# Kernel optimization log

Hardware: AMD Instinct MI355X
Metric: run time of the kernel (lower is better)

The kernel has to match this reference:

```python
import jax, jax.numpy as jnp
import numpy as np

EPS = 1e-6


def setup_inputs() -> dict:
    key = jax.random.key(0)
    k1, k2, k3, k4 = jax.random.split(key, 4)
    B, N, D = 8, 4096, 512
    x = jax.random.normal(k1, (B, N, D), dtype=jnp.float32)
    # torch nn.Linear(dim, 3*dim, bias=False): weight shape [3D, D], y = x @ W.T
    w_qkv = jax.random.normal(k2, (3 * D, D), dtype=jnp.float32) * (1.0 / np.sqrt(D))
    w_proj = jax.random.normal(k3, (D, D), dtype=jnp.float32) * (1.0 / np.sqrt(D))
    b_proj = jax.random.normal(k4, (D,), dtype=jnp.float32) * 0.01
    return {"x": x, "w_qkv": w_qkv, "w_proj": w_proj, "b_proj": b_proj, "heads": 8}


def reference(x, w_qkv, w_proj, b_proj, heads):
    B, N, D = x.shape
    H = heads
    d = D // H
    # qkv projection -> (3, B, H, N, d)
    qkv = (x @ w_qkv.T).reshape(B, N, 3, H, d).transpose(2, 0, 3, 1, 4)
    q, k, v = qkv[0], qkv[1], qkv[2]
    # elu+1 feature map (positive features)
    q = jax.nn.elu(q) + 1.0 + EPS
    k = jax.nn.elu(k) + 1.0 + EPS
    # kv summary: [B,H,d,d]
    kv = jnp.einsum('bhnd,bhne->bhde', k, v)
    # denominator: q . sum_n(k) -> [B,H,N]
    denom = jnp.einsum('bhnd,bhd->bhn', q, k.sum(axis=2))
    out = jnp.einsum('bhnd,bhde->bhne', q, kv) / (denom[..., None] + EPS)
    out = out.transpose(0, 2, 1, 3).reshape(B, N, D)
    return out @ w_proj.T + b_proj
```

## Files before the change

kernel.cpp:

```cpp
#include <hip/hip_runtime.h>
#include <hip/hip_bf16.h>
#include <math.h>

#define EPSF 1e-6f

constexpr int Bc = 8;
constexpr int Nc = 4096;
constexpr int Dc = 512;
constexpr int QKVC = 3 * Dc;

typedef __attribute__((ext_vector_type(8))) short short8v;
typedef __attribute__((ext_vector_type(8))) unsigned short ushort8v;
typedef __attribute__((ext_vector_type(4))) float float4v;

__device__ __forceinline__ unsigned short f2bf(float f) {
    union { float f; unsigned int u; } v; v.f = f;
    unsigned int u = v.u;
    return (unsigned short)((u + 0x7fffu + ((u >> 16) & 1u)) >> 16);
}
__device__ __forceinline__ float bf2f(unsigned short h) {
    union { unsigned int u; float f; } v; v.u = ((unsigned int)h) << 16;
    return v.f;
}

typedef __attribute__((address_space(1))) const void gvoid_t;
typedef __attribute__((address_space(3))) void lvoid_t;
__device__ __forceinline__ void llds16(const void* g, void* l) {
    __builtin_amdgcn_global_load_lds((gvoid_t*)g, (lvoid_t*)l, 16, 0, 0);
}

__global__ __launch_bounds__(256) void cvt_f32_bf16(
    const float* __restrict__ in, unsigned short* __restrict__ out, int n8)
{
    int i = blockIdx.x * 256 + threadIdx.x;
    if (i >= n8) return;
    float4 a = reinterpret_cast<const float4*>(in)[2 * i];
    float4 b = reinterpret_cast<const float4*>(in)[2 * i + 1];
    ushort8v o;
    o[0] = f2bf(a.x); o[1] = f2bf(a.y); o[2] = f2bf(a.z); o[3] = f2bf(a.w);
    o[4] = f2bf(b.x); o[5] = f2bf(b.y); o[6] = f2bf(b.z); o[7] = f2bf(b.w);
    reinterpret_cast<ushort8v*>(out)[i] = o;
}

__global__ __launch_bounds__(256) void cvt_weights(
    const float* __restrict__ wq, const float* __restrict__ wp,
    unsigned short* __restrict__ wqo, unsigned short* __restrict__ wpo)
{
    const int i = blockIdx.x * 256 + threadIdx.x;
    const int NQ = 1536 * 512 / 8;
    const float* src; unsigned short* dst; int idx;
    if (i < NQ) { src = wq; dst = wqo; idx = i; }
    else        { src = wp; dst = wpo; idx = i - NQ; }
    float4 a = reinterpret_cast<const float4*>(src)[2 * idx];
    float4 b = reinterpret_cast<const float4*>(src)[2 * idx + 1];
    ushort8v o;
    o[0] = f2bf(a.x); o[1] = f2bf(a.y); o[2] = f2bf(a.z); o[3] = f2bf(a.w);
    o[4] = f2bf(b.x); o[5] = f2bf(b.y); o[6] = f2bf(b.z); o[7] = f2bf(b.w);
    reinterpret_cast<ushort8v*>(dst)[idx] = o;
}

__global__ __launch_bounds__(512, 2) void gemm_qkv(
    const unsigned short* __restrict__ A,
    const unsigned short* __restrict__ Bm,
    unsigned short* __restrict__ Cout)
{
    constexpr int LDA = 512, LDB = 512, LDC = 1536;
    constexpr int NT = 8;
    __shared__ unsigned short ring[3][24576];

    const int t = threadIdx.x;
    const int orig = blockIdx.x;
    const int wg = (orig & 7) * 192 + (orig >> 3);
    const int bm = (wg / 12) * 256;
    const int bn = (wg % 12) * 128;

    const int w = t >> 6, lane = t & 63;
    const int ln = lane & 15, g = lane >> 4;
    const int wr = (w >> 1) * 64;
    const int wc = (w & 1) * 64;
    const int l7 = ln & 7;

    const int rs = t >> 3;
    const int ci = t & 7;
    const int swz = ci ^ (rs & 7);
    const unsigned short* As0 = A + (size_t)(bm + rs) * LDA + swz * 8;
    const unsigned short* As1 = A + (size_t)(bm + 64 + rs) * LDA + swz * 8;
    const unsigned short* As2 = A + (size_t)(bm + 128 + rs) * LDA + swz * 8;
    const unsigned short* As3 = A + (size_t)(bm + 192 + rs) * LDA + swz * 8;
    const unsigned short* Bs0 = Bm + (size_t)(bn + rs) * LDB + swz * 8;
    const unsigned short* Bs1 = Bm + (size_t)(bn + 64 + rs) * LDB + swz * 8;

#define STAGEQ(Tt) do {                                                        \
        const int k0_ = (Tt) * 64;                                             \
        unsigned short* dA_ = &ring[(Tt) % 3][0];                              \
        unsigned short* dB_ = &ring[(Tt) % 3][16384];                          \
        llds16(As0 + k0_, dA_ + (size_t)t * 8);                                \
        llds16(As1 + k0_, dA_ + (size_t)(512 + t) * 8);                        \
        llds16(As2 + k0_, dA_ + (size_t)(1024 + t) * 8);                       \
        llds16(As3 + k0_, dA_ + (size_t)(1536 + t) * 8);                       \
        llds16(Bs0 + k0_, dB_ + (size_t)t * 8);                                \
        llds16(Bs1 + k0_, dB_ + (size_t)(512 + t) * 8);                        \
    } while (0)

    float4v acc[4][4];
#pragma unroll
    for (int i = 0; i < 4; ++i)
#pragma unroll
        for (int j = 0; j < 4; ++j) acc[i][j] = {0.f, 0.f, 0.f, 0.f};

    STAGEQ(0);
    STAGEQ(1);
    asm volatile("s_waitcnt vmcnt(6)" ::: "memory");
    __builtin_amdgcn_s_barrier();
    __builtin_amdgcn_sched_barrier(0);

#pragma unroll
    for (int T = 0; T < NT; ++T) {
        if (T + 2 < NT) STAGEQ(T + 2);

        const unsigned short* base = &ring[T % 3][0];
        short8v a[4][2], b[4][2];
#pragma unroll
        for (int i = 0; i < 4; ++i)
#pragma unroll
            for (int kk = 0; kk < 2; ++kk) {
                const int row = wr + i * 16 + ln;
                a[i][kk] = *reinterpret_cast<const short8v*>(
                    base + row * 64 + (((kk * 4 + g) ^ l7) << 3));
            }
#pragma unroll
        for (int j = 0; j < 4; ++j)
#pragma unroll
            for (int kk = 0; kk < 2; ++kk) {
                const int row = wc + j * 16 + ln;
                b[j][kk] = *reinterpret_cast<const short8v*>(
                    base + 16384 + row * 64 + (((kk * 4 + g) ^ l7) << 3));
            }

        __builtin_amdgcn_s_setprio(1);
#pragma unroll
        for (int kk = 0; kk < 2; ++kk)
#pragma unroll
            for (int i = 0; i < 4; ++i)
#pragma unroll
                for (int j = 0; j < 4; ++j)
                    acc[i][j] = __builtin_amdgcn_mfma_f32_16x16x32_bf16(
                        a[i][kk], b[j][kk], acc[i][j], 0, 0, 0);
        __builtin_amdgcn_s_setprio(0);

        if (T + 1 < NT) {
            if (T + 2 < NT)
                asm volatile("s_waitcnt vmcnt(6)" ::: "memory");
            else
                asm volatile("s_waitcnt vmcnt(0)" ::: "memory");
            __builtin_amdgcn_s_barrier();
            __builtin_amdgcn_sched_barrier(0);
        }
    }
#undef STAGEQ

#pragma unroll
    for (int i = 0; i < 4; ++i) {
        const int Rb = bm + wr + i * 16 + g * 4;
#pragma unroll
        for (int j = 0; j < 4; ++j) {
            const int Cc = bn + wc + j * 16 + ln;
            const bool do_elu = (Cc < 1024);
#pragma unroll
            for (int r = 0; r < 4; ++r) {
                float v = acc[i][j][r];
                if (do_elu) v = (v > 0.f) ? (v + 1.0f + EPSF) : (expf(v) + EPSF);
                Cout[(size_t)(Rb + r) * LDC + Cc] = f2bf(v);
            }
        }
    }
}

__global__ __launch_bounds__(256) void kv_part(
    const unsigned short* __restrict__ qkv,
    float* __restrict__ kvp, float* __restrict__ ksp)
{
    const int bh = blockIdx.x, chunk = blockIdx.y;
    const int b = bh >> 3, h = bh & 7;

    __shared__ float ktT[4096];
    __shared__ float vtT[4096];
    __shared__ float ksl[16][64];

    const int t = threadIdx.x;
    const int di = t >> 4, ej = t & 15;
    const bool isK = (t < 128);
    const int ts = isK ? t : t - 128;
    const int slot = ts & 7;
    const int ng = ts >> 3;

    const size_t base = ((size_t)b * Nc + (size_t)chunk * 512) * QKVC + h * 64
                      + (isK ? Dc : 2 * Dc) + slot * 8;

    float acc[4][4] = {};
    float ks8[8] = {};

    for (int it = 0; it < 8; ++it) {
        {
            const unsigned short* src = qkv + base + (size_t)(it * 64 + 4 * ng) * QKVC;
            ushort8v r0 = *reinterpret_cast<const ushort8v*>(src);
            ushort8v r1 = *reinterpret_cast<const ushort8v*>(src + QKVC);
            ushort8v r2 = *reinterpret_cast<const ushort8v*>(src + 2 * QKVC);
            ushort8v r3 = *reinterpret_cast<const ushort8v*>(src + 3 * QKVC);
            float* dst = isK ? ktT : vtT;
#pragma unroll
            for (int i = 0; i < 8; ++i) {
                const int row = 8 * slot + i;
                float4 wv = make_float4(bf2f(r0[i]), bf2f(r1[i]), bf2f(r2[i]), bf2f(r3[i]));
                *reinterpret_cast<float4*>(dst + row * 64 + ((ng ^ (row & 15)) << 2)) = wv;
                if (isK) ks8[i] += wv.x + wv.y + wv.z + wv.w;
            }
        }
        __syncthreads();

#pragma unroll 4
        for (int nc = 0; nc < 16; ++nc) {
            float4 kd[4], ve[4];
#pragma unroll
            for (int i = 0; i < 4; ++i)
                kd[i] = *reinterpret_cast<const float4*>(
                    ktT + (di + 16 * i) * 64 + ((nc ^ di) << 2));
#pragma unroll
            for (int j = 0; j < 4; ++j)
                ve[j] = *reinterpret_cast<const float4*>(
                    vtT + (ej + 16 * j) * 64 + ((nc ^ ej) << 2));
#pragma unroll
            for (int i = 0; i < 4; ++i)
#pragma unroll
                for (int j = 0; j < 4; ++j) {
                    acc[i][j] += kd[i].x * ve[j].x;
                    acc[i][j] += kd[i].y * ve[j].y;
                    acc[i][j] += kd[i].z * ve[j].z;
                    acc[i][j] += kd[i].w * ve[j].w;
                }
        }
        __syncthreads();
    }

    float* kvpp = kvp + ((size_t)bh * 8 + chunk) * 4096;
#pragma unroll
    for (int i = 0; i < 4; ++i)
#pragma unroll
        for (int j = 0; j < 4; ++j)
            kvpp[(di + 16 * i) * 64 + (ej + 16 * j)] = acc[i][j];

    if (isK) {
#pragma unroll
        for (int i = 0; i < 8; ++i) ksl[ng][8 * slot + i] = ks8[i];
    }
    __syncthreads();
    if (t < 64) {
        float s = 0.f;
#pragma unroll
        for (int c = 0; c < 16; ++c) s += ksl[c][t];
        ksp[((size_t)bh * 8 + chunk) * 64 + t] = s;
    }
}

__global__ __launch_bounds__(256) void kv_reduce(
    const float* __restrict__ kvp, const float* __restrict__ ksp,
    unsigned short* __restrict__ kvb, float* __restrict__ ksum)
{
    const int bh = blockIdx.x, t = threadIdx.x;
    const float* src = kvp + (size_t)bh * 8 * 4096;
#pragma unroll
    for (int i = 0; i < 16; ++i) {
        const int idx = i * 256 + t;
        float s = 0.f;
#pragma unroll
        for (int c = 0; c < 8; ++c) s += src[c * 4096 + idx];
        kvb[(size_t)bh * 4096 + idx] = f2bf(s);
    }
    if (t < 64) {
        float s = 0.f;
#pragma unroll
        for (int c = 0; c < 8; ++c) s += ksp[((size_t)bh * 8 + c) * 64 + t];
        ksum[bh * 64 + t] = s;
    }
}

__global__ __launch_bounds__(256) void gemm_M(
    const unsigned short* __restrict__ kvb,
    const unsigned short* __restrict__ wp,
    unsigned short* __restrict__ MT)
{
    const int bh = blockIdx.x, b = bh >> 3, h = bh & 7;
    const int t = threadIdx.x, w = t >> 6, lane = t & 63;
    const int ln = lane & 15, g = lane >> 4;

    float4v acc[8][4];
#pragma unroll
    for (int i = 0; i < 8; ++i)
#pragma unroll
        for (int j = 0; j < 4; ++j) acc[i][j] = {0.f, 0.f, 0.f, 0.f};

#pragma unroll
    for (int kk = 0; kk < 2; ++kk) {
        short8v a[8], bf[4];
#pragma unroll
        for (int i = 0; i < 8; ++i)
            a[i] = *reinterpret_cast<const short8v*>(
                wp + (size_t)(w * 128 + i * 16 + ln) * 512 + h * 64 + kk * 32 + g * 8);
#pragma unroll
        for (int j = 0; j < 4; ++j)
            bf[j] = *reinterpret_cast<const short8v*>(
                kvb + (size_t)bh * 4096 + (j * 16 + ln) * 64 + kk * 32 + g * 8);
#pragma unroll
        for (int i = 0; i < 8; ++i)
#pragma unroll
            for (int j = 0; j < 4; ++j)
                acc[i][j] = __builtin_amdgcn_mfma_f32_16x16x32_bf16(a[i], bf[j], acc[i][j], 0, 0, 0);
    }

#pragma unroll
    for (int i = 0; i < 8; ++i) {
        const int c0 = w * 128 + i * 16 + g * 4;
#pragma unroll
        for (int j = 0; j < 4; ++j) {
            const int d = j * 16 + ln;
#pragma unroll
            for (int r = 0; r < 4; ++r)
                MT[(size_t)b * 262144 + (size_t)(c0 + r) * 512 + h * 64 + d] =
                    f2bf(acc[i][j][r]);
        }
    }
}

__global__ __launch_bounds__(256) void q_scale(
    unsigned short* __restrict__ qkv, const float* __restrict__ ksum)
{
    __shared__ float kss[512];
    const int blk = blockIdx.x;
    const int b = blk >> 7;
    const int t = threadIdx.x;
    kss[t] = ksum[b * 512 + t];
    kss[t + 256] = ksum[b * 512 + 256 + t];
    __syncthreads();

    const int row = blk * 32 + (t >> 3);
    const int h = t & 7;
    unsigned short* p = qkv + (size_t)row * QKVC + h * 64;

    ushort8v v[8];
#pragma unroll
    for (int s = 0; s < 8; ++s) v[s] = *reinterpret_cast<const ushort8v*>(p + s * 8);

    float den = EPSF;
#pragma unroll
    for (int s = 0; s < 8; ++s)
#pragma unroll
        for (int m = 0; m < 8; ++m)
            den += bf2f(v[s][m]) * kss[h * 64 + s * 8 + m];
    const float inv = 1.0f / den;

#pragma unroll
    for (int s = 0; s < 8; ++s) {
        ushort8v o;
#pragma unroll
        for (int m = 0; m < 8; ++m) o[m] = f2bf(bf2f(v[s][m]) * inv);
        *reinterpret_cast<ushort8v*>(p + s * 8) = o;
    }
}

__global__ __launch_bounds__(512, 2) void gemm_out(
    const unsigned short* __restrict__ A,
    const unsigned short* __restrict__ Bt,
    const float* __restrict__ bias,
    float* __restrict__ out)
{
    constexpr int LDA = 1536, LDB = 512, NT = 8;
    __shared__ unsigned short ring[3][24576];

    const int t = threadIdx.x;
    const int orig = blockIdx.x;
    const int wg = (orig & 7) * 64 + (orig >> 3);
    const int bm = (wg >> 2) * 256;
    const int bn = (wg & 3) * 128;
    const unsigned short* Bm = Bt + (size_t)(bm >> 12) * 262144;

    const int w = t >> 6, lane = t & 63;
    const int ln = lane & 15, g = lane >> 4;
    const int wr = (w >> 1) * 64;
    const int wc = (w & 1) * 64;
    const int l7 = ln & 7;

    const int rs = t >> 3;
    const int ci = t & 7;
    const int swz = ci ^ (rs & 7);
    const unsigned short* As0 = A + (size_t)(bm + rs) * LDA + swz * 8;
    const unsigned short* As1 = A + (size_t)(bm + 64 + rs) * LDA + swz * 8;
    const unsigned short* As2 = A + (size_t)(bm + 128 + rs) * LDA + swz * 8;
    const unsigned short* As3 = A + (size_t)(bm + 192 + rs) * LDA + swz * 8;
    const unsigned short* Bs0 = Bm + (size_t)(bn + rs) * LDB + swz * 8;
    const unsigned short* Bs1 = Bm + (size_t)(bn + 64 + rs) * LDB + swz * 8;

#define STAGEO(Tt) do {                                                        \
        const int k0_ = (Tt) * 64;                                             \
        unsigned short* dA_ = &ring[(Tt) % 3][0];                              \
        unsigned short* dB_ = &ring[(Tt) % 3][16384];                          \
        llds16(As0 + k0_, dA_ + (size_t)t * 8);                                \
        llds16(As1 + k0_, dA_ + (size_t)(512 + t) * 8);                        \
        llds16(As2 + k0_, dA_ + (size_t)(1024 + t) * 8);                       \
        llds16(As3 + k0_, dA_ + (size_t)(1536 + t) * 8);                       \
        llds16(Bs0 + k0_, dB_ + (size_t)t * 8);                                \
        llds16(Bs1 + k0_, dB_ + (size_t)(512 + t) * 8);                        \
    } while (0)

    float4v acc[4][4];
#pragma unroll
    for (int i = 0; i < 4; ++i)
#pragma unroll
        for (int j = 0; j < 4; ++j) acc[i][j] = {0.f, 0.f, 0.f, 0.f};

    STAGEO(0);
    STAGEO(1);
    asm volatile("s_waitcnt vmcnt(6)" ::: "memory");
    __builtin_amdgcn_s_barrier();
    __builtin_amdgcn_sched_barrier(0);

#pragma unroll
    for (int T = 0; T < NT; ++T) {
        if (T + 2 < NT) STAGEO(T + 2);

        const unsigned short* base = &ring[T % 3][0];
        short8v a[4][2], b[4][2];
#pragma unroll
        for (int i = 0; i < 4; ++i)
#pragma unroll
            for (int kk = 0; kk < 2; ++kk) {
                const int row = wr + i * 16 + ln;
                a[i][kk] = *reinterpret_cast<const short8v*>(
                    base + row * 64 + (((kk * 4 + g) ^ l7) << 3));
            }
#pragma unroll
        for (int j = 0; j < 4; ++j)
#pragma unroll
            for (int kk = 0; kk < 2; ++kk) {
                const int row = wc + j * 16 + ln;
                b[j][kk] = *reinterpret_cast<const short8v*>(
                    base + 16384 + row * 64 + (((kk * 4 + g) ^ l7) << 3));
            }

        __builtin_amdgcn_s_setprio(1);
#pragma unroll
        for (int kk = 0; kk < 2; ++kk)
#pragma unroll
            for (int i = 0; i < 4; ++i)
#pragma unroll
                for (int j = 0; j < 4; ++j)
                    acc[i][j] = __builtin_amdgcn_mfma_f32_16x16x32_bf16(
                        a[i][kk], b[j][kk], acc[i][j], 0, 0, 0);
        __builtin_amdgcn_s_setprio(0);

        if (T + 1 < NT) {
            if (T + 2 < NT)
                asm volatile("s_waitcnt vmcnt(6)" ::: "memory");
            else
                asm volatile("s_waitcnt vmcnt(0)" ::: "memory");
            __builtin_amdgcn_s_barrier();
            __builtin_amdgcn_sched_barrier(0);
        }
    }
#undef STAGEO

#pragma unroll
    for (int i = 0; i < 4; ++i) {
        const int Rb = bm + wr + i * 16 + g * 4;
#pragma unroll
        for (int j = 0; j < 4; ++j) {
            const int Cc = bn + wc + j * 16 + ln;
            const float bv = bias[Cc];
#pragma unroll
            for (int r = 0; r < 4; ++r)
                out[(size_t)(Rb + r) * 512 + Cc] = acc[i][j][r] + bv;
        }
    }
}

extern "C" void kernel_launch(void* const* d_in, const int* in_sizes, int n_in,
                              void* d_out, int out_size, void* d_ws, size_t ws_size,
                              hipStream_t stream)
{
    const float* x      = (const float*)d_in[0];
    const float* w_qkv  = (const float*)d_in[1];
    const float* w_proj = (const float*)d_in[2];
    const float* b_proj = (const float*)d_in[3];
    float* out = (float*)d_out;

    char* ws = (char*)d_ws;
    unsigned short* qkvb = (unsigned short*)ws;
    size_t off = (size_t)32768 * 1536 * 2;
    unsigned short* xb   = (unsigned short*)(ws + off); off += (size_t)32768 * 512 * 2;
    unsigned short* wqb  = (unsigned short*)(ws + off); off += (size_t)1536 * 512 * 2;
    unsigned short* wpb  = (unsigned short*)(ws + off); off += (size_t)512 * 512 * 2;
    float* kvp           = (float*)(ws + off);          off += (size_t)64 * 8 * 4096 * 4;
    float* ksp           = (float*)(ws + off);          off += (size_t)64 * 8 * 64 * 4;
    unsigned short* kvb  = (unsigned short*)(ws + off); off += (size_t)64 * 4096 * 2;
    float* ksumb         = (float*)(ws + off);          off += (size_t)64 * 64 * 4;
    unsigned short* MT   = (unsigned short*)(ws + off); off += (size_t)8 * 512 * 512 * 2;

    cvt_f32_bf16<<<dim3((32768 * 512 / 8 + 255) / 256), dim3(256), 0, stream>>>(x, xb, 32768 * 512 / 8);
    cvt_weights<<<dim3(((1536 * 512 + 512 * 512) / 8 + 255) / 256), dim3(256), 0, stream>>>(
        w_qkv, w_proj, wqb, wpb);

    gemm_qkv<<<dim3(1536), dim3(512), 0, stream>>>(xb, wqb, qkvb);

    kv_part<<<dim3(64, 8), dim3(256), 0, stream>>>(qkvb, kvp, ksp);
    kv_reduce<<<dim3(64), dim3(256), 0, stream>>>(kvp, ksp, kvb, ksumb);

    gemm_M<<<dim3(64), dim3(256), 0, stream>>>(kvb, wpb, MT);

    q_scale<<<dim3(1024), dim3(256), 0, stream>>>(qkvb, ksumb);

    gemm_out<<<dim3(512), dim3(512), 0, stream>>>(qkvb, MT, b_proj, out);
}
```

Baseline: 199.0 us.

## Compute kv partial products with bf16 MFMA instead of scalar FMA

The kv_part kernel now stores K and V tiles in shared memory as bf16, with padded rows in place of float XOR-swizzled rows. Each wavefront computes a 16x64 slice of the 64x64 K^T V partial using mfma_f32_16x16x32_bf16 rather than a 4x4-per-thread FP32 outer-product loop. This halves the LDS footprint and removes the scalar FMA work. Numerics should match closely, since the inputs were already bf16 and accumulation stays in fp32. kv_part is only one of several kernels, so its share of total time limits the gain.

```diff
diff --git a/kernel.cpp b/kernel.cpp
--- a/kernel.cpp
+++ b/kernel.cpp
@@ -183,21 +183,27 @@
     const int bh = blockIdx.x, chunk = blockIdx.y;
     const int b = bh >> 3, h = bh & 7;
 
-    __shared__ float ktT[4096];
-    __shared__ float vtT[4096];
+    __shared__ unsigned short ktT[64 * 72];
+    __shared__ unsigned short vtT[64 * 72];
     __shared__ float ksl[16][64];
 
     const int t = threadIdx.x;
-    const int di = t >> 4, ej = t & 15;
+    const int w = t >> 6, lane = t & 63;
+    const int ln = lane & 15, g = lane >> 4;
+
     const bool isK = (t < 128);
     const int ts = isK ? t : t - 128;
     const int slot = ts & 7;
     const int ng = ts >> 3;
 
     const size_t base = ((size_t)b * Nc + (size_t)chunk * 512) * QKVC + h * 64
-                      + (isK ? Dc : 2 * Dc) + slot * 8;
-
-    float acc[4][4] = {};
+                      + (isK ? Dc : 2 * Dc) + (size_t)slot * 8;
+
+    unsigned short* Tdst = isK ? ktT : vtT;
+
+    float4v acc[4];
+#pragma unroll
+    for (int j = 0; j < 4; ++j) acc[j] = {0.f, 0.f, 0.f, 0.f};
     float ks8[8] = {};
 
     for (int it = 0; it < 8; ++it) {
@@ -207,47 +213,45 @@
             ushort8v r1 = *reinterpret_cast<const ushort8v*>(src + QKVC);
             ushort8v r2 = *reinterpret_cast<const ushort8v*>(src + 2 * QKVC);
             ushort8v r3 = *reinterpret_cast<const ushort8v*>(src + 3 * QKVC);
-            float* dst = isK ? ktT : vtT;
 #pragma unroll
             for (int i = 0; i < 8; ++i) {
-                const int row = 8 * slot + i;
-                float4 wv = make_float4(bf2f(r0[i]), bf2f(r1[i]), bf2f(r2[i]), bf2f(r3[i]));
-                *reinterpret_cast<float4*>(dst + row * 64 + ((ng ^ (row & 15)) << 2)) = wv;
-                if (isK) ks8[i] += wv.x + wv.y + wv.z + wv.w;
+                const int d = 8 * slot + i;
+                unsigned long long pk = (unsigned long long)r0[i]
+                    | ((unsigned long long)r1[i] << 16)
+                    | ((unsigned long long)r2[i] << 32)
+                    | ((unsigned long long)r3[i] << 48);
+                *reinterpret_cast<unsigned long long*>(&Tdst[d * 72 + 4 * ng]) = pk;
+                if (isK) ks8[i] += bf2f(r0[i]) + bf2f(r1[i]) + bf2f(r2[i]) + bf2f(r3[i]);
             }
         }
         __syncthreads();
 
-#pragma unroll 4
-        for (int nc = 0; nc < 16; ++nc) {
-            float4 kd[4], ve[4];
-#pragma unroll
-            for (int i = 0; i < 4; ++i)
-                kd[i] = *reinterpret_cast<const float4*>(
-                    ktT + (di + 16 * i) * 64 + ((nc ^ di) << 2));
+        short8v afr[2], bfr[4][2];
+#pragma unroll
+        for (int kk = 0; kk < 2; ++kk)
+            afr[kk] = *reinterpret_cast<const short8v*>(
+                &ktT[(w * 16 + ln) * 72 + kk * 32 + g * 8]);
+#pragma unroll
+        for (int j = 0; j < 4; ++j)
+#pragma unroll
+            for (int kk = 0; kk < 2; ++kk)
+                bfr[j][kk] = *reinterpret_cast<const short8v*>(
+                    &vtT[(j * 16 + ln) * 72 + kk * 32 + g * 8]);
+#pragma unroll
+        for (int kk = 0; kk < 2; ++kk)
 #pragma unroll
             for (int j = 0; j < 4; ++j)
-                ve[j] = *reinterpret_cast<const float4*>(
-                    vtT + (ej + 16 * j) * 64 + ((nc ^ ej) << 2));
-#pragma unroll
-            for (int i = 0; i < 4; ++i)
-#pragma unroll
-                for (int j = 0; j < 4; ++j) {
-                    acc[i][j] += kd[i].x * ve[j].x;
-                    acc[i][j] += kd[i].y * ve[j].y;
-                    acc[i][j] += kd[i].z * ve[j].z;
-                    acc[i][j] += kd[i].w * ve[j].w;
-                }
-        }
+                acc[j] = __builtin_amdgcn_mfma_f32_16x16x32_bf16(
+                    afr[kk], bfr[j][kk], acc[j], 0, 0, 0);
         __syncthreads();
     }
 
     float* kvpp = kvp + ((size_t)bh * 8 + chunk) * 4096;
 #pragma unroll
-    for (int i = 0; i < 4; ++i)
-#pragma unroll
-        for (int j = 0; j < 4; ++j)
-            kvpp[(di + 16 * i) * 64 + (ej + 16 * j)] = acc[i][j];
+    for (int j = 0; j < 4; ++j)
+#pragma unroll
+        for (int r = 0; r < 4; ++r)
+            kvpp[(w * 16 + g * 4 + r) * 64 + j * 16 + ln] = acc[j][r];
 
     if (isK) {
 #pragma unroll
```

Result: faster. 166.2 us, median of 2 (-16.5%).
